# Kernel tuning notes

Measured on AMD Instinct MI355X. Metric: run time of the kernel, lower is better.

The kernel has to match this reference:

```python
import jax, jax.numpy as jnp
import numpy as np

N = 5000
NUM_CLASSES = 81
BBOX_STD = jnp.array([0.1, 0.1, 0.2, 0.2], dtype=jnp.float32)
MIN_CONF = 0.7
MAX_INST = 100
NMS_THR = 0.3


def apply_box_delta(boxes, deltas):
    # boxes: [N,4] (y1,x1,y2,x2); deltas: [N,4] (dy,dx,log(dh),log(dw))
    h = boxes[:, 2] - boxes[:, 0]
    w = boxes[:, 3] - boxes[:, 1]
    cy = boxes[:, 0] + 0.5 * h
    cx = boxes[:, 1] + 0.5 * w
    cy = cy + deltas[:, 0] * h
    cx = cx + deltas[:, 1] * w
    h = h * jnp.exp(deltas[:, 2])
    w = w * jnp.exp(deltas[:, 3])
    y1 = cy - 0.5 * h
    x1 = cx - 0.5 * w
    return jnp.stack([y1, x1, y1 + h, x1 + w], axis=1)


def clip_boxes(boxes, window):
    wy1, wx1, wy2, wx2 = window[0], window[1], window[2], window[3]
    y1 = jnp.clip(boxes[:, 0], wy1, wy2)
    x1 = jnp.clip(boxes[:, 1], wx1, wx2)
    y2 = jnp.clip(boxes[:, 2], wy1, wy2)
    x2 = jnp.clip(boxes[:, 3], wx1, wx2)
    return jnp.stack([y1, x1, y2, x2], axis=1)


def pairwise_iou(boxes):
    # boxes: [N,4] -> iou: [N,N]
    y1, x1, y2, x2 = boxes[:, 0], boxes[:, 1], boxes[:, 2], boxes[:, 3]
    area = jnp.maximum(y2 - y1, 0.0) * jnp.maximum(x2 - x1, 0.0)
    iy1 = jnp.maximum(y1[:, None], y1[None, :])
    ix1 = jnp.maximum(x1[:, None], x1[None, :])
    iy2 = jnp.minimum(y2[:, None], y2[None, :])
    ix2 = jnp.minimum(x2[:, None], x2[None, :])
    inter = jnp.maximum(iy2 - iy1, 0.0) * jnp.maximum(ix2 - ix1, 0.0)
    union = area[:, None] + area[None, :] - inter
    return jnp.where(union > 0.0, inter / jnp.maximum(union, 1e-12), 0.0)


def setup_inputs() -> dict:
    key = jax.random.key(0)
    k1, k2, k3 = jax.random.split(key, 3)
    # valid boxes in normalized coords: (y1,x1) = min corner, (y2,x2) = max corner
    pts = jax.random.uniform(k1, (N, 2, 2), dtype=jnp.float32)
    lo = jnp.min(pts, axis=1)  # [N,2] -> (ymin, xmin)
    hi = jnp.max(pts, axis=1)  # [N,2] -> (ymax, xmax)
    ROIs = jnp.concatenate([lo, hi], axis=1)
    probs = jax.random.uniform(k2, (N, NUM_CLASSES), dtype=jnp.float32)
    deltas = jax.random.normal(k3, (N, NUM_CLASSES, 4), dtype=jnp.float32) * 0.5
    window = jnp.array([0.0, 0.0, 1.0, 1.0], dtype=jnp.float32)
    return {"ROIs": ROIs, "probs": probs, "deltas": deltas, "window": window}


def reference(ROIs, probs, deltas, window):
    n = probs.shape[0]
    rows = jnp.arange(n)
    # compute_delta: top class per ROI, its score and class-specific delta
    class_ids = jnp.argmax(probs, axis=1)
    class_scores = probs[rows, class_ids]
    deltas_specific = deltas[rows, class_ids] * BBOX_STD
    # refine + clip
    refined = clip_boxes(apply_box_delta(ROIs, deltas_specific), window)
    # keep: non-background & above confidence threshold
    valid = (class_ids > 0) & (class_scores >= MIN_CONF)
    # per-class greedy NMS, processed in global descending-score order
    # (identical result to per-unique-class tf.image.non_max_suppression)
    iou = pairwise_iou(refined)  # [N,N]
    neg_inf = jnp.float32(-jnp.inf)
    order = jnp.argsort(-jnp.where(valid, class_scores, neg_inf))

    def step(carry, i):
        kept, counts = carry
        c = class_ids[i]
        suppressed = jnp.any(kept & (class_ids == c) & (iou[i] > NMS_THR))
        ok = valid[i] & (~suppressed) & (counts[c] < MAX_INST)
        kept = kept.at[i].set(ok)
        counts = counts.at[c].add(ok.astype(jnp.int32))
        return (kept, counts), None

    init = (jnp.zeros((n,), dtype=bool), jnp.zeros((NUM_CLASSES,), dtype=jnp.int32))
    (kept, _), _ = jax.lax.scan(step, init, order)
    final = valid & kept
    # top detection_max_instances by score among surviving boxes
    masked_scores = jnp.where(final, class_scores, neg_inf)
    top_scores, top_ids = jax.lax.top_k(masked_scores, MAX_INST)
    ok = top_scores > neg_inf
    det = jnp.concatenate(
        [refined[top_ids],
         class_ids[top_ids].astype(jnp.float32)[:, None],
         class_scores[top_ids][:, None]], axis=1)
    # zero_pad_detections: invalid slots are zero
    return jnp.where(ok[:, None], det, 0.0)  # [MAX_INST, 6]
```

## Files before the change

kernel.cpp:

```cpp
#include <hip/hip_runtime.h>
#include <math.h>

#define NROI 5000
#define NCLS 81
#define MIN_CONF_F 0.7f
#define MAX_INST_I 100
#define NMS_THR_F 0.3f

__global__ __launch_bounds__(256) void det_stage1(
    const float* __restrict__ rois, const float* __restrict__ probs,
    const float* __restrict__ deltas, const float* __restrict__ window,
    float4* __restrict__ g_box, float* __restrict__ g_score,
    int* __restrict__ g_cid, int* __restrict__ g_kept)
{
  const int gtid = blockIdx.x * blockDim.x + threadIdx.x;
  const int i = gtid >> 6;
  const int lane = threadIdx.x & 63;
  if (i >= NROI) return;
  const float* p = probs + (size_t)i * NCLS;
  float v0 = p[lane];
  unsigned long long key =
      ((unsigned long long)__float_as_uint(v0) << 32) | (unsigned)(255 - lane);
  if (lane < NCLS - 64) {
    float v1 = p[64 + lane];
    unsigned long long k1 =
        ((unsigned long long)__float_as_uint(v1) << 32) | (unsigned)(255 - (64 + lane));
    if (k1 > key) key = k1;
  }
  #pragma unroll
  for (int off = 32; off > 0; off >>= 1) {
    unsigned long long o = __shfl_xor(key, off, 64);
    if (o > key) key = o;
  }
  if (lane == 0) {
    int bc = 255 - (int)(key & 0xFFull);
    float best = __uint_as_float((unsigned)(key >> 32));
    const float* d = deltas + ((size_t)i * NCLS + bc) * 4;
    float dy = d[0]*0.1f, dx = d[1]*0.1f, dh = d[2]*0.2f, dwv = d[3]*0.2f;
    float y1 = rois[i*4+0], x1 = rois[i*4+1], y2 = rois[i*4+2], x2 = rois[i*4+3];
    float h = y2 - y1, w = x2 - x1;
    float cy = y1 + 0.5f*h, cx = x1 + 0.5f*w;
    cy = cy + dy*h; cx = cx + dx*w;
    h = h*expf(dh); w = w*expf(dwv);
    float ny1 = cy - 0.5f*h, nx1 = cx - 0.5f*w;
    float ny2 = ny1 + h, nx2 = nx1 + w;
    float wy1 = window[0], wx1 = window[1], wy2 = window[2], wx2 = window[3];
    ny1 = fminf(fmaxf(ny1, wy1), wy2);
    nx1 = fminf(fmaxf(nx1, wx1), wx2);
    ny2 = fminf(fmaxf(ny2, wy1), wy2);
    nx2 = fminf(fmaxf(nx2, wx1), wx2);
    g_box[i] = make_float4(ny1, nx1, ny2, nx2);
    g_score[i] = best;
    g_cid[i] = (bc > 0 && best >= MIN_CONF_F) ? bc : -1;
    g_kept[i] = 0;
  }
}

#define CAP2 128
__global__ __launch_bounds__(256) void det_stage2(
    const float4* __restrict__ g_box, const float* __restrict__ g_score,
    const int* __restrict__ g_cid, int* __restrict__ g_kept)
{
  const int c = blockIdx.x + 1;
  const int tid = threadIdx.x;
  __shared__ int scnt;
  __shared__ unsigned long long keys[CAP2], skey[CAP2];
  __shared__ float by1[CAP2], bx1[CAP2], by2[CAP2], bx2[CAP2], barea[CAP2];
  __shared__ unsigned int mask[CAP2][4];
  __shared__ unsigned char skept[CAP2];
  if (tid == 0) scnt = 0;
  for (int q = tid; q < CAP2 * 4; q += 256) ((unsigned int*)mask)[q] = 0u;
  if (tid < CAP2) skept[tid] = 0;
  __syncthreads();
  const int4* cid4 = (const int4*)g_cid;
  for (int v = tid; v < NROI / 4; v += 256) {
    int4 cv = cid4[v];
    int base = v * 4;
    #pragma unroll
    for (int q = 0; q < 4; ++q) {
      int cq = (q == 0) ? cv.x : (q == 1) ? cv.y : (q == 2) ? cv.z : cv.w;
      if (cq == c) {
        int i = base + q;
        int pos = atomicAdd(&scnt, 1);
        if (pos < CAP2) {
          unsigned int sb = __float_as_uint(g_score[i]);
          keys[pos] = ((unsigned long long)sb << 32) |
                      (unsigned int)(0xFFFFFFFFu - (unsigned int)i);
        }
      }
    }
  }
  __syncthreads();
  int cnt = scnt < CAP2 ? scnt : CAP2;
  if (cnt == 0) return;
  if (tid < cnt) {
    unsigned long long mk = keys[tid];
    int r = 0;
    for (int q = 0; q < cnt; ++q) r += (keys[q] > mk) ? 1 : 0;
    skey[r] = mk;
  }
  __syncthreads();
  if (tid < cnt) {
    int idx = (int)(0xFFFFFFFFu - (unsigned)(skey[tid] & 0xFFFFFFFFull));
    float4 b = g_box[idx];
    by1[tid] = b.x; bx1[tid] = b.y; by2[tid] = b.z; bx2[tid] = b.w;
    barea[tid] = fmaxf(b.z - b.x, 0.0f) * fmaxf(b.w - b.y, 0.0f);
  }
  __syncthreads();
  int m = 1, lg = 0;
  while (m < cnt) { m <<= 1; ++lg; }
  int tot = m * m;
  for (int p = tid; p < tot; p += 256) {
    int j = p >> lg, k = p & (m - 1);
    if (k > j && k < cnt && j < cnt) {
      float iy1 = fmaxf(by1[j], by1[k]);
      float ix1 = fmaxf(bx1[j], bx1[k]);
      float iy2 = fminf(by2[j], by2[k]);
      float ix2 = fminf(bx2[j], bx2[k]);
      float inter = fmaxf(iy2 - iy1, 0.0f) * fmaxf(ix2 - ix1, 0.0f);
      float uni = barea[j] + barea[k] - inter;
      float iou = (uni > 0.0f) ? inter / fmaxf(uni, 1e-12f) : 0.0f;
      if (iou > NMS_THR_F) atomicOr(&mask[j][k >> 5], 1u << (k & 31));
    }
  }
  __syncthreads();
  if (tid == 0) {
    unsigned long long rlo = 0ull, rhi = 0ull;
    int kc = 0;
    for (int j = 0; j < cnt; ++j) {
      unsigned int w0 = mask[j][0], w1 = mask[j][1], w2 = mask[j][2], w3 = mask[j][3];
      bool sup = (j < 64) ? (((rlo >> j) & 1ull) != 0)
                          : (((rhi >> (j - 64)) & 1ull) != 0);
      if (!sup && kc < MAX_INST_I) {
        skept[j] = 1; ++kc;
        rlo |= (unsigned long long)w0 | ((unsigned long long)w1 << 32);
        rhi |= (unsigned long long)w2 | ((unsigned long long)w3 << 32);
      }
    }
  }
  __syncthreads();
  if (tid < cnt && skept[tid]) {
    int idx = (int)(0xFFFFFFFFu - (unsigned)(skey[tid] & 0xFFFFFFFFull));
    g_kept[idx] = 1;
  }
}

#define HBINS 2048
#define CAP3 2048
#define BMIN 0x3F333
__global__ __launch_bounds__(1024) void det_stage3(
    const float4* __restrict__ g_box, const float* __restrict__ g_score,
    const int* __restrict__ g_cid, const int* __restrict__ g_kept,
    float* __restrict__ out)
{
  const int tid = threadIdx.x;
  __shared__ int hist[HBINS];
  __shared__ unsigned long long keys[CAP3];
  __shared__ int wsum[16];
  __shared__ float orows[6 * MAX_INST_I];
  __shared__ int scnt, sR;
  for (int b = tid; b < HBINS; b += 1024) hist[b] = 0;
  if (tid == 0) { scnt = 0; sR = 1 << 30; }
  if (tid < 6 * MAX_INST_I) orows[tid] = 0.0f;
  __syncthreads();
  const int4* k4 = (const int4*)g_kept;
  for (int v = tid; v < NROI / 4; v += 1024) {
    int4 kv = k4[v];
    int base = 4 * v;
    #pragma unroll
    for (int q = 0; q < 4; ++q) {
      int kq = (q == 0) ? kv.x : (q == 1) ? kv.y : (q == 2) ? kv.z : kv.w;
      if (kq) {
        unsigned int bits = __float_as_uint(g_score[base + q]);
        int b = (int)(bits >> 12) - BMIN;
        b = b < 0 ? 0 : (b > HBINS - 1 ? HBINS - 1 : b);
        atomicAdd(&hist[b], 1);
      }
    }
  }
  __syncthreads();
  int a0 = hist[HBINS - 1 - 2 * tid];
  int a1 = hist[HBINS - 2 - 2 * tid];
  int val = a0 + a1;
  int incl = val;
  const int lane = tid & 63, wv = tid >> 6;
  #pragma unroll
  for (int off = 1; off < 64; off <<= 1) {
    int n = __shfl_up(incl, off, 64);
    if (lane >= off) incl += n;
  }
  if (lane == 63) wsum[wv] = incl;
  __syncthreads();
  if (tid == 0) {
    int s = 0;
    for (int q = 0; q < 16; ++q) { s += wsum[q]; wsum[q] = s; }
  }
  __syncthreads();
  incl += (wv > 0) ? wsum[wv - 1] : 0;
  int excl = incl - val;
  int c0 = excl + a0;
  int c1 = incl;
  if (c0 >= MAX_INST_I) atomicMin(&sR, 2 * tid);
  else if (c1 >= MAX_INST_I) atomicMin(&sR, 2 * tid + 1);
  __syncthreads();
  const int T = (sR >= HBINS) ? 0 : (HBINS - 1 - sR);
  for (int v = tid; v < NROI / 4; v += 1024) {
    int4 kv = k4[v];
    int base = 4 * v;
    #pragma unroll
    for (int q = 0; q < 4; ++q) {
      int kq = (q == 0) ? kv.x : (q == 1) ? kv.y : (q == 2) ? kv.z : kv.w;
      if (kq) {
        int i = base + q;
        unsigned int bits = __float_as_uint(g_score[i]);
        int b = (int)(bits >> 12) - BMIN;
        b = b < 0 ? 0 : (b > HBINS - 1 ? HBINS - 1 : b);
        if (b >= T) {
          int pos = atomicAdd(&scnt, 1);
          if (pos < CAP3)
            keys[pos] = ((unsigned long long)bits << 32) |
                        (unsigned int)(0xFFFFFFFFu - (unsigned int)i);
        }
      }
    }
  }
  __syncthreads();
  int cnt = scnt < CAP3 ? scnt : CAP3;
  if (tid < cnt) {
    unsigned long long mk = keys[tid];
    int r = 0;
    for (int q = 0; q < cnt; ++q) r += (keys[q] > mk) ? 1 : 0;
    if (r < MAX_INST_I) {
      int idx = (int)(0xFFFFFFFFu - (unsigned)(mk & 0xFFFFFFFFull));
      float4 b = g_box[idx];
      orows[r * 6 + 0] = b.x;
      orows[r * 6 + 1] = b.y;
      orows[r * 6 + 2] = b.z;
      orows[r * 6 + 3] = b.w;
      orows[r * 6 + 4] = (float)g_cid[idx];
      orows[r * 6 + 5] = g_score[idx];
    }
  }
  __syncthreads();
  if (tid < 6 * MAX_INST_I) out[tid] = orows[tid];
}

extern "C" void kernel_launch(void* const* d_in, const int* in_sizes, int n_in,
                              void* d_out, int out_size, void* d_ws, size_t ws_size,
                              hipStream_t stream)
{
  const float* rois   = (const float*)d_in[0];
  const float* probs  = (const float*)d_in[1];
  const float* deltas = (const float*)d_in[2];
  const float* window = (const float*)d_in[3];
  float* out = (float*)d_out;

  char* ws = (char*)d_ws;
  float4* g_box  = (float4*)ws;
  float*  g_score = (float*)(ws + 80000);
  int*    g_cid   = (int*)(ws + 100000);
  int*    g_kept  = (int*)(ws + 120000);

  det_stage1<<<(NROI * 64 + 255) / 256, 256, 0, stream>>>(rois, probs, deltas, window,
                                                          g_box, g_score, g_cid, g_kept);
  det_stage2<<<NCLS - 1, 256, 0, stream>>>(g_box, g_score, g_cid, g_kept);
  det_stage3<<<1, 1024, 0, stream>>>(g_box, g_score, g_cid, g_kept, out);
}
```

Measured before the change: 98.50 us.

## Fuse per-class NMS and final top-k via last-block ticket and survivor list

Merges the per-class NMS kernel and the single-block top-k kernel into one launch. Each class block appends its kept boxes to a compact global survivor list, and the last block to finish (found through an atomic ticket) builds the histogram and ranks candidates over that list only, not all 5000 ROIs. This removes one kernel launch and the full scan of a kept-flag array, and it drops the per-ROI zeroing of that array. In exchange the final top-k runs on a 256-thread block instead of 1024 threads, and correctness now depends on global atomics plus threadfence ordering.

```diff
diff --git a/kernel.cpp b/kernel.cpp
--- a/kernel.cpp
+++ b/kernel.cpp
@@ -6,14 +6,20 @@
 #define MIN_CONF_F 0.7f
 #define MAX_INST_I 100
 #define NMS_THR_F 0.3f
+#define CAP2 128
+#define SURV_CAP 8192
+#define HBINS 2048
+#define CAPF 512
+#define BMIN 0x3F333
 
 __global__ __launch_bounds__(256) void det_stage1(
     const float* __restrict__ rois, const float* __restrict__ probs,
     const float* __restrict__ deltas, const float* __restrict__ window,
     float4* __restrict__ g_box, float* __restrict__ g_score,
-    int* __restrict__ g_cid, int* __restrict__ g_kept)
+    int* __restrict__ g_cid, unsigned int* __restrict__ ctrl)
 {
   const int gtid = blockIdx.x * blockDim.x + threadIdx.x;
+  if (gtid == 0) { ctrl[0] = 0u; ctrl[1] = 0u; }
   const int i = gtid >> 6;
   const int lane = threadIdx.x & 63;
   if (i >= NROI) return;
@@ -52,14 +58,14 @@
     g_box[i] = make_float4(ny1, nx1, ny2, nx2);
     g_score[i] = best;
     g_cid[i] = (bc > 0 && best >= MIN_CONF_F) ? bc : -1;
-    g_kept[i] = 0;
   }
 }
 
-#define CAP2 128
-__global__ __launch_bounds__(256) void det_stage2(
+__global__ __launch_bounds__(256) void det_nms_topk(
     const float4* __restrict__ g_box, const float* __restrict__ g_score,
-    const int* __restrict__ g_cid, int* __restrict__ g_kept)
+    const int* __restrict__ g_cid, unsigned int* __restrict__ ctrl,
+    unsigned long long* __restrict__ surv_key, int* __restrict__ surv_cid,
+    float* __restrict__ out)
 {
   const int c = blockIdx.x + 1;
   const int tid = threadIdx.x;
@@ -68,6 +74,14 @@
   __shared__ float by1[CAP2], bx1[CAP2], by2[CAP2], bx2[CAP2], barea[CAP2];
   __shared__ unsigned int mask[CAP2][4];
   __shared__ unsigned char skept[CAP2];
+  __shared__ int sticket;
+  __shared__ int hist[HBINS];
+  __shared__ unsigned long long cand[CAPF];
+  __shared__ int csrc[CAPF];
+  __shared__ float orows[6 * MAX_INST_I];
+  __shared__ int wsum[4];
+  __shared__ int fcnt, sR;
+
   if (tid == 0) scnt = 0;
   for (int q = tid; q < CAP2 * 4; q += 256) ((unsigned int*)mask)[q] = 0u;
   if (tid < CAP2) skept[tid] = 0;
@@ -92,157 +106,132 @@
   }
   __syncthreads();
   int cnt = scnt < CAP2 ? scnt : CAP2;
-  if (cnt == 0) return;
-  if (tid < cnt) {
-    unsigned long long mk = keys[tid];
-    int r = 0;
-    for (int q = 0; q < cnt; ++q) r += (keys[q] > mk) ? 1 : 0;
-    skey[r] = mk;
-  }
-  __syncthreads();
-  if (tid < cnt) {
-    int idx = (int)(0xFFFFFFFFu - (unsigned)(skey[tid] & 0xFFFFFFFFull));
-    float4 b = g_box[idx];
-    by1[tid] = b.x; bx1[tid] = b.y; by2[tid] = b.z; bx2[tid] = b.w;
-    barea[tid] = fmaxf(b.z - b.x, 0.0f) * fmaxf(b.w - b.y, 0.0f);
-  }
-  __syncthreads();
-  int m = 1, lg = 0;
-  while (m < cnt) { m <<= 1; ++lg; }
-  int tot = m * m;
-  for (int p = tid; p < tot; p += 256) {
-    int j = p >> lg, k = p & (m - 1);
-    if (k > j && k < cnt && j < cnt) {
-      float iy1 = fmaxf(by1[j], by1[k]);
-      float ix1 = fmaxf(bx1[j], bx1[k]);
-      float iy2 = fminf(by2[j], by2[k]);
-      float ix2 = fminf(bx2[j], bx2[k]);
-      float inter = fmaxf(iy2 - iy1, 0.0f) * fmaxf(ix2 - ix1, 0.0f);
-      float uni = barea[j] + barea[k] - inter;
-      float iou = (uni > 0.0f) ? inter / fmaxf(uni, 1e-12f) : 0.0f;
-      if (iou > NMS_THR_F) atomicOr(&mask[j][k >> 5], 1u << (k & 31));
+  if (cnt > 0) {
+    if (tid < cnt) {
+      unsigned long long mk = keys[tid];
+      int r = 0;
+      for (int q = 0; q < cnt; ++q) r += (keys[q] > mk) ? 1 : 0;
+      skey[r] = mk;
+    }
+    __syncthreads();
+    if (tid < cnt) {
+      int idx = (int)(0xFFFFFFFFu - (unsigned)(skey[tid] & 0xFFFFFFFFull));
+      float4 b = g_box[idx];
+      by1[tid] = b.x; bx1[tid] = b.y; by2[tid] = b.z; bx2[tid] = b.w;
+      barea[tid] = fmaxf(b.z - b.x, 0.0f) * fmaxf(b.w - b.y, 0.0f);
+    }
+    __syncthreads();
+    int m = 1, lg = 0;
+    while (m < cnt) { m <<= 1; ++lg; }
+    int tot = m * m;
+    for (int p = tid; p < tot; p += 256) {
+      int j = p >> lg, k = p & (m - 1);
+      if (k > j && k < cnt) {
+        float iy1 = fmaxf(by1[j], by1[k]);
+        float ix1 = fmaxf(bx1[j], bx1[k]);
+        float iy2 = fminf(by2[j], by2[k]);
+        float ix2 = fminf(bx2[j], bx2[k]);
+        float inter = fmaxf(iy2 - iy1, 0.0f) * fmaxf(ix2 - ix1, 0.0f);
+        float uni = barea[j] + barea[k] - inter;
+        float iou = (uni > 0.0f) ? inter / fmaxf(uni, 1e-12f) : 0.0f;
+        if (iou > NMS_THR_F) atomicOr(&mask[j][k >> 5], 1u << (k & 31));
+      }
+    }
+    __syncthreads();
+    if (tid == 0) {
+      unsigned long long rlo = 0ull, rhi = 0ull;
+      int kc = 0;
+      for (int j = 0; j < cnt; ++j) {
+        unsigned int w0 = mask[j][0], w1 = mask[j][1], w2 = mask[j][2], w3 = mask[j][3];
+        bool sup = (j < 64) ? (((rlo >> j) & 1ull) != 0)
+                            : (((rhi >> (j - 64)) & 1ull) != 0);
+        if (!sup && kc < MAX_INST_I) {
+          skept[j] = 1; ++kc;
+          rlo |= (unsigned long long)w0 | ((unsigned long long)w1 << 32);
+          rhi |= (unsigned long long)w2 | ((unsigned long long)w3 << 32);
+        }
+      }
+    }
+    __syncthreads();
+    if (tid < cnt && skept[tid]) {
+      unsigned int pos = atomicAdd(&ctrl[0], 1u);
+      if (pos < SURV_CAP) { surv_key[pos] = skey[tid]; surv_cid[pos] = c; }
     }
   }
   __syncthreads();
   if (tid == 0) {
-    unsigned long long rlo = 0ull, rhi = 0ull;
-    int kc = 0;
-    for (int j = 0; j < cnt; ++j) {
-      unsigned int w0 = mask[j][0], w1 = mask[j][1], w2 = mask[j][2], w3 = mask[j][3];
-      bool sup = (j < 64) ? (((rlo >> j) & 1ull) != 0)
-                          : (((rhi >> (j - 64)) & 1ull) != 0);
-      if (!sup && kc < MAX_INST_I) {
-        skept[j] = 1; ++kc;
-        rlo |= (unsigned long long)w0 | ((unsigned long long)w1 << 32);
-        rhi |= (unsigned long long)w2 | ((unsigned long long)w3 << 32);
-      }
-    }
-  }
-  __syncthreads();
-  if (tid < cnt && skept[tid]) {
-    int idx = (int)(0xFFFFFFFFu - (unsigned)(skey[tid] & 0xFFFFFFFFull));
-    g_kept[idx] = 1;
-  }
-}
-
-#define HBINS 2048
-#define CAP3 2048
-#define BMIN 0x3F333
-__global__ __launch_bounds__(1024) void det_stage3(
-    const float4* __restrict__ g_box, const float* __restrict__ g_score,
-    const int* __restrict__ g_cid, const int* __restrict__ g_kept,
-    float* __restrict__ out)
-{
-  const int tid = threadIdx.x;
-  __shared__ int hist[HBINS];
-  __shared__ unsigned long long keys[CAP3];
-  __shared__ int wsum[16];
-  __shared__ float orows[6 * MAX_INST_I];
-  __shared__ int scnt, sR;
-  for (int b = tid; b < HBINS; b += 1024) hist[b] = 0;
-  if (tid == 0) { scnt = 0; sR = 1 << 30; }
-  if (tid < 6 * MAX_INST_I) orows[tid] = 0.0f;
-  __syncthreads();
-  const int4* k4 = (const int4*)g_kept;
-  for (int v = tid; v < NROI / 4; v += 1024) {
-    int4 kv = k4[v];
-    int base = 4 * v;
-    #pragma unroll
-    for (int q = 0; q < 4; ++q) {
-      int kq = (q == 0) ? kv.x : (q == 1) ? kv.y : (q == 2) ? kv.z : kv.w;
-      if (kq) {
-        unsigned int bits = __float_as_uint(g_score[base + q]);
-        int b = (int)(bits >> 12) - BMIN;
-        b = b < 0 ? 0 : (b > HBINS - 1 ? HBINS - 1 : b);
-        atomicAdd(&hist[b], 1);
-      }
-    }
-  }
-  __syncthreads();
-  int a0 = hist[HBINS - 1 - 2 * tid];
-  int a1 = hist[HBINS - 2 - 2 * tid];
-  int val = a0 + a1;
+    __threadfence();
+    sticket = (int)atomicAdd(&ctrl[1], 1u);
+  }
+  __syncthreads();
+  if (sticket != NCLS - 2) return;
+  __threadfence();
+
+  unsigned int n = atomicAdd(&ctrl[0], 0u);
+  if (n > SURV_CAP) n = SURV_CAP;
+  for (int b = tid; b < HBINS; b += 256) hist[b] = 0;
+  if (tid == 0) { fcnt = 0; sR = 1 << 30; }
+  for (int q = tid; q < 6 * MAX_INST_I; q += 256) orows[q] = 0.0f;
+  __syncthreads();
+  for (unsigned int i = tid; i < n; i += 256) {
+    unsigned int bits = (unsigned int)(surv_key[i] >> 32);
+    int b = (int)(bits >> 12) - BMIN;
+    b = b < 0 ? 0 : (b > HBINS - 1 ? HBINS - 1 : b);
+    atomicAdd(&hist[b], 1);
+  }
+  __syncthreads();
+  int a[8]; int val = 0;
+  #pragma unroll
+  for (int q = 0; q < 8; ++q) { a[q] = hist[HBINS - 1 - (8 * tid + q)]; val += a[q]; }
   int incl = val;
   const int lane = tid & 63, wv = tid >> 6;
   #pragma unroll
   for (int off = 1; off < 64; off <<= 1) {
-    int n = __shfl_up(incl, off, 64);
-    if (lane >= off) incl += n;
+    int nn = __shfl_up(incl, off, 64);
+    if (lane >= off) incl += nn;
   }
   if (lane == 63) wsum[wv] = incl;
   __syncthreads();
-  if (tid == 0) {
-    int s = 0;
-    for (int q = 0; q < 16; ++q) { s += wsum[q]; wsum[q] = s; }
-  }
+  if (tid == 0) { int s = 0; for (int q = 0; q < 4; ++q) { s += wsum[q]; wsum[q] = s; } }
   __syncthreads();
   incl += (wv > 0) ? wsum[wv - 1] : 0;
-  int excl = incl - val;
-  int c0 = excl + a0;
-  int c1 = incl;
-  if (c0 >= MAX_INST_I) atomicMin(&sR, 2 * tid);
-  else if (c1 >= MAX_INST_I) atomicMin(&sR, 2 * tid + 1);
+  int run = incl - val;
+  #pragma unroll
+  for (int q = 0; q < 8; ++q) {
+    run += a[q];
+    if (run >= MAX_INST_I) { atomicMin(&sR, 8 * tid + q); break; }
+  }
   __syncthreads();
   const int T = (sR >= HBINS) ? 0 : (HBINS - 1 - sR);
-  for (int v = tid; v < NROI / 4; v += 1024) {
-    int4 kv = k4[v];
-    int base = 4 * v;
-    #pragma unroll
-    for (int q = 0; q < 4; ++q) {
-      int kq = (q == 0) ? kv.x : (q == 1) ? kv.y : (q == 2) ? kv.z : kv.w;
-      if (kq) {
-        int i = base + q;
-        unsigned int bits = __float_as_uint(g_score[i]);
-        int b = (int)(bits >> 12) - BMIN;
-        b = b < 0 ? 0 : (b > HBINS - 1 ? HBINS - 1 : b);
-        if (b >= T) {
-          int pos = atomicAdd(&scnt, 1);
-          if (pos < CAP3)
-            keys[pos] = ((unsigned long long)bits << 32) |
-                        (unsigned int)(0xFFFFFFFFu - (unsigned int)i);
-        }
-      }
-    }
-  }
-  __syncthreads();
-  int cnt = scnt < CAP3 ? scnt : CAP3;
-  if (tid < cnt) {
-    unsigned long long mk = keys[tid];
+  for (unsigned int i = tid; i < n; i += 256) {
+    unsigned long long k = surv_key[i];
+    unsigned int bits = (unsigned int)(k >> 32);
+    int b = (int)(bits >> 12) - BMIN;
+    b = b < 0 ? 0 : (b > HBINS - 1 ? HBINS - 1 : b);
+    if (b >= T) {
+      int pos = atomicAdd(&fcnt, 1);
+      if (pos < CAPF) { cand[pos] = k; csrc[pos] = (int)i; }
+    }
+  }
+  __syncthreads();
+  int fc = fcnt < CAPF ? fcnt : CAPF;
+  for (int e = tid; e < fc; e += 256) {
+    unsigned long long mk = cand[e];
     int r = 0;
-    for (int q = 0; q < cnt; ++q) r += (keys[q] > mk) ? 1 : 0;
+    for (int q = 0; q < fc; ++q) r += (cand[q] > mk) ? 1 : 0;
     if (r < MAX_INST_I) {
-      int idx = (int)(0xFFFFFFFFu - (unsigned)(mk & 0xFFFFFFFFull));
-      float4 b = g_box[idx];
+      int roi = (int)(0xFFFFFFFFu - (unsigned)(mk & 0xFFFFFFFFull));
+      float4 b = g_box[roi];
       orows[r * 6 + 0] = b.x;
       orows[r * 6 + 1] = b.y;
       orows[r * 6 + 2] = b.z;
       orows[r * 6 + 3] = b.w;
-      orows[r * 6 + 4] = (float)g_cid[idx];
-      orows[r * 6 + 5] = g_score[idx];
-    }
-  }
-  __syncthreads();
-  if (tid < 6 * MAX_INST_I) out[tid] = orows[tid];
+      orows[r * 6 + 4] = (float)surv_cid[csrc[e]];
+      orows[r * 6 + 5] = __uint_as_float((unsigned int)(mk >> 32));
+    }
+  }
+  __syncthreads();
+  for (int q = tid; q < 6 * MAX_INST_I; q += 256) out[q] = orows[q];
 }
 
 extern "C" void kernel_launch(void* const* d_in, const int* in_sizes, int n_in,
@@ -256,13 +245,15 @@
   float* out = (float*)d_out;
 
   char* ws = (char*)d_ws;
-  float4* g_box  = (float4*)ws;
+  float4* g_box   = (float4*)ws;
   float*  g_score = (float*)(ws + 80000);
   int*    g_cid   = (int*)(ws + 100000);
-  int*    g_kept  = (int*)(ws + 120000);
-
-  det_stage1<<<(NROI * 64 + 255) / 256, 256, 0, stream>>>(rois, probs, deltas, window,
-                                                          g_box, g_score, g_cid, g_kept);
-  det_stage2<<<NCLS - 1, 256, 0, stream>>>(g_box, g_score, g_cid, g_kept);
-  det_stage3<<<1, 1024, 0, stream>>>(g_box, g_score, g_cid, g_kept, out);
+  unsigned int* ctrl = (unsigned int*)(ws + 120000);
+  unsigned long long* surv_key = (unsigned long long*)(ws + 120064);
+  int* surv_cid = (int*)(ws + 120064 + SURV_CAP * 8);
+
+  det_stage1<<<(NROI * 64 + 255) / 256, 256, 0, stream>>>(
+      rois, probs, deltas, window, g_box, g_score, g_cid, ctrl);
+  det_nms_topk<<<NCLS - 1, 256, 0, stream>>>(
+      g_box, g_score, g_cid, ctrl, surv_key, surv_cid, out);
 }
```

Result: slower. 102.6 us (+4.1%).
